# Kernel optimization log

Measured on AMD Instinct MI355X. Metric: run time of the kernel, lower is better.

Reference implementation:

```python
import jax, jax.numpy as jnp
import numpy as np

B = 2_000_000
ND = 3

def _skew(v):
    # v: [B,3] -> [B,3,3] skew-symmetric matrix
    z = jnp.zeros_like(v[..., 0])
    r0 = jnp.stack([z, -v[..., 2], v[..., 1]], axis=-1)
    r1 = jnp.stack([v[..., 2], z, -v[..., 0]], axis=-1)
    r2 = jnp.stack([-v[..., 1], v[..., 0], z], axis=-1)
    return jnp.stack([r0, r1, r2], axis=-2)

def _rotmat(v):
    # Closed-form expm of skew(v) (Rodrigues). Mathematically identical to tf.linalg.expm.
    th2 = jnp.sum(v * v, axis=-1)                      # [B]
    th = jnp.sqrt(th2)
    small = th < 1e-6
    th_s = jnp.where(small, 1.0, th)
    th2_s = jnp.where(small, 1.0, th2)
    a = jnp.where(small, 1.0, jnp.sin(th) / th_s)      # sin(t)/t
    b = jnp.where(small, 0.5, (1.0 - jnp.cos(th)) / th2_s)  # (1-cos t)/t^2
    K = _skew(v)                                       # [B,3,3]
    I = jnp.eye(ND, dtype=v.dtype)
    return I + a[:, None, None] * K + b[:, None, None] * jnp.matmul(K, K)

def setup_inputs() -> dict:
    key = jax.random.key(0)
    k1, k2, k3, k4 = jax.random.split(key, 4)
    trans = jax.random.normal(k1, (B, ND), dtype=jnp.float32)
    rotat = jax.random.normal(k2, (B, ND), dtype=jnp.float32)
    scal_dir = jax.random.normal(k3, (B, ND), dtype=jnp.float32)
    scal = jax.random.normal(k4, (B, ND), dtype=jnp.float32)
    return {"trans": trans, "rotat": rotat, "scal_dir": scal_dir, "scal": scal}

def reference(trans, rotat, scal_dir, scal):
    R = _rotmat(rotat)          # [B,3,3] rotation
    U = _rotmat(scal_dir)       # [B,3,3] scaling direction
    D = jnp.exp(scal)           # expm(diag(s)) == diag(exp(s)), [B,3]
    # U @ diag(D) @ U^T, then R @ (.)
    Ut = jnp.swapaxes(U, -1, -2)
    M = jnp.matmul(U, D[:, :, None] * Ut)   # diag(D) @ U^T broadcast as row-scaling
    M = jnp.matmul(R, M)
    return jnp.concatenate([M, trans[:, :, None]], axis=2)  # [B,3,4]
```

## Files before the change

kernel.cpp:

```cpp
#include <hip/hip_runtime.h>
#include <math.h>

#define TPB 256

__device__ __forceinline__ void rodrigues(float v0, float v1, float v2, float R[9]) {
    float th2 = v0 * v0 + v1 * v1 + v2 * v2;
    float th  = sqrtf(th2);
    float s, c;
    sincosf(th, &s, &c);
    bool  sm = th < 1e-6f;
    float a  = sm ? 1.0f : s / th;
    float b  = sm ? 0.5f : (1.0f - c) / th2;
    float cc = 1.0f - b * th2;
    R[0] = cc + b * v0 * v0;      R[1] = b * v0 * v1 - a * v2;  R[2] = b * v0 * v2 + a * v1;
    R[3] = b * v0 * v1 + a * v2;  R[4] = cc + b * v1 * v1;      R[5] = b * v1 * v2 - a * v0;
    R[6] = b * v0 * v2 - a * v1;  R[7] = b * v1 * v2 + a * v0;  R[8] = cc + b * v2 * v2;
}

__global__ __launch_bounds__(TPB) void aff_kernel(
    const float4* __restrict__ trans,
    const float4* __restrict__ rotat,
    const float4* __restrict__ sdir,
    const float4* __restrict__ scal,
    float4* __restrict__ out,
    int B)
{
    __shared__ float s_in[4][TPB * 3];

    const int tid  = threadIdx.x;
    const int base = blockIdx.x * TPB;
    const int n    = min(TPB, B - base);
    const int nf4  = (n * 3) >> 2;

    if (tid < nf4) {
        const int gbase = (base * 3) >> 2;
        float4 a = trans[gbase + tid];
        float4 b = rotat[gbase + tid];
        float4 c = sdir [gbase + tid];
        float4 d = scal [gbase + tid];
        ((float4*)&s_in[0][0])[tid] = a;
        ((float4*)&s_in[1][0])[tid] = b;
        ((float4*)&s_in[2][0])[tid] = c;
        ((float4*)&s_in[3][0])[tid] = d;
    }
    __syncthreads();

    if (tid < n) {
        float t0 = s_in[0][3*tid+0], t1 = s_in[0][3*tid+1], t2 = s_in[0][3*tid+2];

        float R[9], U[9];
        rodrigues(s_in[1][3*tid+0], s_in[1][3*tid+1], s_in[1][3*tid+2], R);
        rodrigues(s_in[2][3*tid+0], s_in[2][3*tid+1], s_in[2][3*tid+2], U);
        const float d0 = expf(s_in[3][3*tid+0]);
        const float d1 = expf(s_in[3][3*tid+1]);
        const float d2 = expf(s_in[3][3*tid+2]);

        const float W0 = U[0]*d0, W1 = U[1]*d1, W2 = U[2]*d2;
        const float W3 = U[3]*d0, W4 = U[4]*d1, W5 = U[5]*d2;
        const float W6 = U[6]*d0, W7 = U[7]*d1, W8 = U[8]*d2;

        const float S00 = W0*U[0] + W1*U[1] + W2*U[2];
        const float S01 = W0*U[3] + W1*U[4] + W2*U[5];
        const float S02 = W0*U[6] + W1*U[7] + W2*U[8];
        const float S11 = W3*U[3] + W4*U[4] + W5*U[5];
        const float S12 = W3*U[6] + W4*U[7] + W5*U[8];
        const float S22 = W6*U[6] + W7*U[7] + W8*U[8];

        const float M00 = R[0]*S00 + R[1]*S01 + R[2]*S02;
        const float M01 = R[0]*S01 + R[1]*S11 + R[2]*S12;
        const float M02 = R[0]*S02 + R[1]*S12 + R[2]*S22;
        const float M10 = R[3]*S00 + R[4]*S01 + R[5]*S02;
        const float M11 = R[3]*S01 + R[4]*S11 + R[5]*S12;
        const float M12 = R[3]*S02 + R[4]*S12 + R[5]*S22;
        const float M20 = R[6]*S00 + R[7]*S01 + R[8]*S02;
        const float M21 = R[6]*S01 + R[7]*S11 + R[8]*S12;
        const float M22 = R[6]*S02 + R[7]*S12 + R[8]*S22;

        float4* o = out + 3 * (base + tid);
        o[0] = make_float4(M00, M01, M02, t0);
        o[1] = make_float4(M10, M11, M12, t1);
        o[2] = make_float4(M20, M21, M22, t2);
    }
}

extern "C" void kernel_launch(void* const* d_in, const int* in_sizes, int n_in,
                              void* d_out, int out_size, void* d_ws, size_t ws_size,
                              hipStream_t stream) {
    int B = in_sizes[0] / 3;
    int blocks = (B + TPB - 1) / TPB;
    aff_kernel<<<blocks, TPB, 0, stream>>>((const float4*)d_in[0], (const float4*)d_in[1],
                                           (const float4*)d_in[2], (const float4*)d_in[3],
                                           (float4*)d_out, B);
}
```

Before: 183.3 us.

## Process four elements per thread with register double-buffered loads, drop LDS staging

Removes the shared-memory staging and block barrier. Each thread now loads its 12-byte rows directly from global memory, and each wave covers 256 elements. Loads for the next element are issued before computing the current one, so memory latency overlaps with the Rodrigues math. The cost is a quarter as many threads, less fully coalesced 12-byte loads, and extra edge-case guards.

```diff
diff --git a/kernel.cpp b/kernel.cpp
--- a/kernel.cpp
+++ b/kernel.cpp
@@ -2,6 +2,8 @@
 #include <math.h>
 
 #define TPB 256
+
+struct __align__(4) f3 { float x, y, z; };
 
 __device__ __forceinline__ void rodrigues(float v0, float v1, float v2, float R[9]) {
     float th2 = v0 * v0 + v1 * v1 + v2 * v2;
@@ -17,78 +19,81 @@
     R[6] = b * v0 * v2 - a * v1;  R[7] = b * v1 * v2 + a * v0;  R[8] = cc + b * v2 * v2;
 }
 
+__device__ __forceinline__ void compute_store(
+    const f3 t, const f3 r, const f3 u, const f3 s, float4* __restrict__ o)
+{
+    float R[9], U[9];
+    rodrigues(r.x, r.y, r.z, R);
+    rodrigues(u.x, u.y, u.z, U);
+    const float d0 = expf(s.x), d1 = expf(s.y), d2 = expf(s.z);
+
+    const float W0 = U[0]*d0, W1 = U[1]*d1, W2 = U[2]*d2;
+    const float W3 = U[3]*d0, W4 = U[4]*d1, W5 = U[5]*d2;
+    const float W6 = U[6]*d0, W7 = U[7]*d1, W8 = U[8]*d2;
+
+    const float S00 = W0*U[0] + W1*U[1] + W2*U[2];
+    const float S01 = W0*U[3] + W1*U[4] + W2*U[5];
+    const float S02 = W0*U[6] + W1*U[7] + W2*U[8];
+    const float S11 = W3*U[3] + W4*U[4] + W5*U[5];
+    const float S12 = W3*U[6] + W4*U[7] + W5*U[8];
+    const float S22 = W6*U[6] + W7*U[7] + W8*U[8];
+
+    const float M00 = R[0]*S00 + R[1]*S01 + R[2]*S02;
+    const float M01 = R[0]*S01 + R[1]*S11 + R[2]*S12;
+    const float M02 = R[0]*S02 + R[1]*S12 + R[2]*S22;
+    const float M10 = R[3]*S00 + R[4]*S01 + R[5]*S02;
+    const float M11 = R[3]*S01 + R[4]*S11 + R[5]*S12;
+    const float M12 = R[3]*S02 + R[4]*S12 + R[5]*S22;
+    const float M20 = R[6]*S00 + R[7]*S01 + R[8]*S02;
+    const float M21 = R[6]*S01 + R[7]*S11 + R[8]*S12;
+    const float M22 = R[6]*S02 + R[7]*S12 + R[8]*S22;
+
+    o[0] = make_float4(M00, M01, M02, t.x);
+    o[1] = make_float4(M10, M11, M12, t.y);
+    o[2] = make_float4(M20, M21, M22, t.z);
+}
+
 __global__ __launch_bounds__(TPB) void aff_kernel(
-    const float4* __restrict__ trans,
-    const float4* __restrict__ rotat,
-    const float4* __restrict__ sdir,
-    const float4* __restrict__ scal,
+    const f3* __restrict__ trans,
+    const f3* __restrict__ rotat,
+    const f3* __restrict__ sdir,
+    const f3* __restrict__ scal,
     float4* __restrict__ out,
     int B)
 {
-    __shared__ float s_in[4][TPB * 3];
+    const int lane  = threadIdx.x & 63;
+    const int wid   = (blockIdx.x * TPB + threadIdx.x) >> 6;
+    const int ebase = wid << 8;
+    if (ebase >= B) return;
 
-    const int tid  = threadIdx.x;
-    const int base = blockIdx.x * TPB;
-    const int n    = min(TPB, B - base);
-    const int nf4  = (n * 3) >> 2;
+    const int e0 = ebase + lane;
+    const bool g1 = (ebase +  64) < B;
+    const bool g2 = (ebase + 128) < B;
+    const bool g3 = (ebase + 192) < B;
 
-    if (tid < nf4) {
-        const int gbase = (base * 3) >> 2;
-        float4 a = trans[gbase + tid];
-        float4 b = rotat[gbase + tid];
-        float4 c = sdir [gbase + tid];
-        float4 d = scal [gbase + tid];
-        ((float4*)&s_in[0][0])[tid] = a;
-        ((float4*)&s_in[1][0])[tid] = b;
-        ((float4*)&s_in[2][0])[tid] = c;
-        ((float4*)&s_in[3][0])[tid] = d;
-    }
-    __syncthreads();
+    f3 tA, rA, uA, sA;
+    f3 tB, rB, uB, sB;
 
-    if (tid < n) {
-        float t0 = s_in[0][3*tid+0], t1 = s_in[0][3*tid+1], t2 = s_in[0][3*tid+2];
+    { const int e = e0;      tA = trans[e]; rA = rotat[e]; uA = sdir[e]; sA = scal[e]; }
+    if (g1) { const int e = e0 + 64;  tB = trans[e]; rB = rotat[e]; uB = sdir[e]; sB = scal[e]; }
 
-        float R[9], U[9];
-        rodrigues(s_in[1][3*tid+0], s_in[1][3*tid+1], s_in[1][3*tid+2], R);
-        rodrigues(s_in[2][3*tid+0], s_in[2][3*tid+1], s_in[2][3*tid+2], U);
-        const float d0 = expf(s_in[3][3*tid+0]);
-        const float d1 = expf(s_in[3][3*tid+1]);
-        const float d2 = expf(s_in[3][3*tid+2]);
+    compute_store(tA, rA, uA, sA, out + 3 * e0);
+    if (g2) { const int e = e0 + 128; tA = trans[e]; rA = rotat[e]; uA = sdir[e]; sA = scal[e]; }
 
-        const float W0 = U[0]*d0, W1 = U[1]*d1, W2 = U[2]*d2;
-        const float W3 = U[3]*d0, W4 = U[4]*d1, W5 = U[5]*d2;
-        const float W6 = U[6]*d0, W7 = U[7]*d1, W8 = U[8]*d2;
+    if (g1) compute_store(tB, rB, uB, sB, out + 3 * (e0 + 64));
+    if (g3) { const int e = e0 + 192; tB = trans[e]; rB = rotat[e]; uB = sdir[e]; sB = scal[e]; }
 
-        const float S00 = W0*U[0] + W1*U[1] + W2*U[2];
-        const float S01 = W0*U[3] + W1*U[4] + W2*U[5];
-        const float S02 = W0*U[6] + W1*U[7] + W2*U[8];
-        const float S11 = W3*U[3] + W4*U[4] + W5*U[5];
-        const float S12 = W3*U[6] + W4*U[7] + W5*U[8];
-        const float S22 = W6*U[6] + W7*U[7] + W8*U[8];
-
-        const float M00 = R[0]*S00 + R[1]*S01 + R[2]*S02;
-        const float M01 = R[0]*S01 + R[1]*S11 + R[2]*S12;
-        const float M02 = R[0]*S02 + R[1]*S12 + R[2]*S22;
-        const float M10 = R[3]*S00 + R[4]*S01 + R[5]*S02;
-        const float M11 = R[3]*S01 + R[4]*S11 + R[5]*S12;
-        const float M12 = R[3]*S02 + R[4]*S12 + R[5]*S22;
-        const float M20 = R[6]*S00 + R[7]*S01 + R[8]*S02;
-        const float M21 = R[6]*S01 + R[7]*S11 + R[8]*S12;
-        const float M22 = R[6]*S02 + R[7]*S12 + R[8]*S22;
-
-        float4* o = out + 3 * (base + tid);
-        o[0] = make_float4(M00, M01, M02, t0);
-        o[1] = make_float4(M10, M11, M12, t1);
-        o[2] = make_float4(M20, M21, M22, t2);
-    }
+    if (g2) compute_store(tA, rA, uA, sA, out + 3 * (e0 + 128));
+    if (g3) compute_store(tB, rB, uB, sB, out + 3 * (e0 + 192));
 }
 
 extern "C" void kernel_launch(void* const* d_in, const int* in_sizes, int n_in,
                               void* d_out, int out_size, void* d_ws, size_t ws_size,
                               hipStream_t stream) {
     int B = in_sizes[0] / 3;
-    int blocks = (B + TPB - 1) / TPB;
-    aff_kernel<<<blocks, TPB, 0, stream>>>((const float4*)d_in[0], (const float4*)d_in[1],
-                                           (const float4*)d_in[2], (const float4*)d_in[3],
+    int waves  = (B + 255) / 256;
+    int blocks = (waves * 64 + TPB - 1) / TPB;
+    aff_kernel<<<blocks, TPB, 0, stream>>>((const f3*)d_in[0], (const f3*)d_in[1],
+                                           (const f3*)d_in[2], (const f3*)d_in[3],
                                            (float4*)d_out, B);
 }
```

New measurement: 184.3 us. No clear change (+0.5%).
